# Optimization experiments

Hardware: AMD Instinct MI355X
Metric: run time of the kernel (lower is better)

Reference implementation:

```python
import jax, jax.numpy as jnp
import numpy as np

N_NODES = 100000
N_EDGES = 500000
HIDDEN = 128


def _layer_norm(h, gamma, beta, eps=1e-5):
    mu = jnp.mean(h, axis=-1, keepdims=True)
    var = jnp.var(h, axis=-1, keepdims=True)
    return (h - mu) * jax.lax.rsqrt(var + eps) * gamma + beta


def setup_inputs() -> dict:
    key = jax.random.key(0)
    ks = jax.random.split(key, 8)
    h = HIDDEN
    x = jax.random.normal(ks[0], (N_NODES, h), dtype=jnp.float32)
    edge_index = jax.random.randint(ks[1], (2, N_EDGES), 0, N_NODES, dtype=jnp.int64)
    edge = jax.random.normal(ks[2], (N_EDGES, h), dtype=jnp.float32)
    # MLP params: Linear(3h -> h), LN, SiLU, Linear(h -> h), LN, Tanh
    W1 = jax.random.normal(ks[3], (3 * h, h), dtype=jnp.float32) * (1.0 / np.sqrt(3 * h))
    b1 = jnp.zeros((h,), dtype=jnp.float32)
    g1 = jnp.ones((h,), dtype=jnp.float32)
    be1 = jnp.zeros((h,), dtype=jnp.float32)
    W2 = jax.random.normal(ks[4], (h, h), dtype=jnp.float32) * (1.0 / np.sqrt(h))
    b2 = jnp.zeros((h,), dtype=jnp.float32)
    g2 = jnp.ones((h,), dtype=jnp.float32)
    be2 = jnp.zeros((h,), dtype=jnp.float32)
    return {"x": x, "edge_index": edge_index, "edge": edge,
            "W1": W1, "b1": b1, "g1": g1, "be1": be1,
            "W2": W2, "b2": b2, "g2": g2, "be2": be2}


def reference(x, edge_index, edge, W1, b1, g1, be1, W2, b2, g2, be2):
    src = edge_index[0]
    dst = edge_index[1]
    # gather src/dst node feats, concat with edge feats -> [E, 3h]
    x_input = jnp.concatenate([x[src], x[dst], edge], axis=-1)
    h1 = jax.nn.silu(_layer_norm(x_input @ W1 + b1, g1, be1))
    h2 = jnp.tanh(_layer_norm(h1 @ W2 + b2, g2, be2))
    return edge + h2
```

## Files before the change

### kernel.cpp

```cpp
#include <hip/hip_runtime.h>

#define E_TOTAL 500000
#define NNODES  100000
#define HID     128
#define K1      384

typedef __bf16 bf16x8 __attribute__((ext_vector_type(8)));
typedef float  f32x4  __attribute__((ext_vector_type(4)));

__global__ void pack_w_kernel(const float* __restrict__ W, __bf16* __restrict__ out, int K) {
    int idx = blockIdx.x * 256 + threadIdx.x;
    if (idx >= K * 128) return;
    int k = idx >> 7, nn = idx & 127;
    int kstep = k >> 5, q = (k >> 3) & 3, j = k & 7;
    int nt = nn >> 4, n15 = nn & 15;
    int lane = q * 16 + n15;
    out[(((kstep * 8 + nt) * 64 + lane) << 3) + j] = (__bf16)W[idx];
}

__launch_bounds__(256, 2)
__global__ void edge_mlp_kernel(
    const float* __restrict__ x,
    const int*   __restrict__ eidx,
    const float* __restrict__ edge,
    const float* __restrict__ b1, const float* __restrict__ g1, const float* __restrict__ be1,
    const float* __restrict__ b2, const float* __restrict__ g2, const float* __restrict__ be2,
    const __bf16* __restrict__ w1f, const __bf16* __restrict__ w2f,
    float* __restrict__ out)
{
    __shared__ __align__(16) __bf16 h1s[4][64][128];

    const int tid  = threadIdx.x;
    const int w    = tid >> 6;
    const int l    = tid & 63;
    const int q    = l >> 4;
    const int n15  = l & 15;
    const int ebase = blockIdx.x * 256 + w * 64;

    const float* psrc[4]; const float* pdst[4]; const float* pedg[4];
    #pragma unroll
    for (int mt = 0; mt < 4; ++mt) {
        int e  = ebase + mt * 16 + n15;
        int ec = e < E_TOTAL ? e : (E_TOTAL - 1);
        int s  = eidx[ec];
        int d  = eidx[E_TOTAL + ec];
        psrc[mt] = x + (size_t)s * HID;
        pdst[mt] = x + (size_t)d * HID;
        pedg[mt] = edge + (size_t)ec * HID;
    }

    f32x4 acc[4][8];
    #pragma unroll
    for (int mt = 0; mt < 4; ++mt)
        #pragma unroll
        for (int nt = 0; nt < 8; ++nt) {
            f32x4 z = {0.f, 0.f, 0.f, 0.f};
            acc[mt][nt] = z;
        }

    #pragma unroll
    for (int ks = 0; ks < 12; ++ks) {
        bf16x8 a[4];
        #pragma unroll
        for (int mt = 0; mt < 4; ++mt) {
            const float* base =
                (ks < 4) ? (psrc[mt] + ks * 32) :
                (ks < 8) ? (pdst[mt] + (ks - 4) * 32) :
                           (pedg[mt] + (ks - 8) * 32);
            base += q * 8;
            float4 v0 = *reinterpret_cast<const float4*>(base);
            float4 v1 = *reinterpret_cast<const float4*>(base + 4);
            bf16x8 t;
            t[0]=(__bf16)v0.x; t[1]=(__bf16)v0.y; t[2]=(__bf16)v0.z; t[3]=(__bf16)v0.w;
            t[4]=(__bf16)v1.x; t[5]=(__bf16)v1.y; t[6]=(__bf16)v1.z; t[7]=(__bf16)v1.w;
            a[mt] = t;
        }
        const bf16x8* wf = reinterpret_cast<const bf16x8*>(w1f) + (size_t)(ks * 8) * 64 + l;
        #pragma unroll
        for (int nt = 0; nt < 8; ++nt) {
            bf16x8 b = wf[nt * 64];
            #pragma unroll
            for (int mt = 0; mt < 4; ++mt)
                acc[mt][nt] = __builtin_amdgcn_mfma_f32_16x16x32_bf16(a[mt], b, acc[mt][nt], 0, 0, 0);
        }
    }

    {
        float b1v[8], g1v[8], be1v[8];
        #pragma unroll
        for (int nt = 0; nt < 8; ++nt) {
            int c = nt * 16 + n15;
            b1v[nt] = b1[c]; g1v[nt] = g1[c]; be1v[nt] = be1[c];
        }
        #pragma unroll
        for (int mt = 0; mt < 4; ++mt) {
            float sm[4] = {0,0,0,0}, sq[4] = {0,0,0,0};
            #pragma unroll
            for (int nt = 0; nt < 8; ++nt)
                #pragma unroll
                for (int r = 0; r < 4; ++r) {
                    float v = acc[mt][nt][r] + b1v[nt];
                    acc[mt][nt][r] = v;
                    sm[r] += v; sq[r] += v * v;
                }
            #pragma unroll
            for (int o = 1; o < 16; o <<= 1)
                #pragma unroll
                for (int r = 0; r < 4; ++r) {
                    sm[r] += __shfl_xor(sm[r], o, 64);
                    sq[r] += __shfl_xor(sq[r], o, 64);
                }
            #pragma unroll
            for (int r = 0; r < 4; ++r) {
                float mu  = sm[r] * (1.f / 128.f);
                float var = sq[r] * (1.f / 128.f) - mu * mu;
                float rs  = rsqrtf(var + 1e-5f);
                int row = mt * 16 + q * 4 + r;
                #pragma unroll
                for (int nt = 0; nt < 8; ++nt) {
                    float v = (acc[mt][nt][r] - mu) * rs * g1v[nt] + be1v[nt];
                    float h = v * (1.f / (1.f + __expf(-v)));
                    int col = nt * 16 + n15;
                    int cb  = (col >> 3) ^ (row & 7);
                    h1s[w][row][cb * 8 + (col & 7)] = (__bf16)h;
                }
            }
        }
    }
    __syncthreads();

    #pragma unroll
    for (int mt = 0; mt < 4; ++mt)
        #pragma unroll
        for (int nt = 0; nt < 8; ++nt) {
            f32x4 z = {0.f, 0.f, 0.f, 0.f};
            acc[mt][nt] = z;
        }
    #pragma unroll
    for (int ks = 0; ks < 4; ++ks) {
        bf16x8 a[4];
        #pragma unroll
        for (int mt = 0; mt < 4; ++mt) {
            int row = mt * 16 + n15;
            int kb  = ks * 4 + q;
            int cb  = kb ^ (row & 7);
            a[mt] = *reinterpret_cast<const bf16x8*>(&h1s[w][row][cb * 8]);
        }
        const bf16x8* wf = reinterpret_cast<const bf16x8*>(w2f) + (size_t)(ks * 8) * 64 + l;
        #pragma unroll
        for (int nt = 0; nt < 8; ++nt) {
            bf16x8 b = wf[nt * 64];
            #pragma unroll
            for (int mt = 0; mt < 4; ++mt)
                acc[mt][nt] = __builtin_amdgcn_mfma_f32_16x16x32_bf16(a[mt], b, acc[mt][nt], 0, 0, 0);
        }
    }

    {
        float b2v[8], g2v[8], be2v[8];
        #pragma unroll
        for (int nt = 0; nt < 8; ++nt) {
            int c = nt * 16 + n15;
            b2v[nt] = b2[c]; g2v[nt] = g2[c]; be2v[nt] = be2[c];
        }
        #pragma unroll
        for (int mt = 0; mt < 4; ++mt) {
            float sm[4] = {0,0,0,0}, sq[4] = {0,0,0,0};
            #pragma unroll
            for (int nt = 0; nt < 8; ++nt)
                #pragma unroll
                for (int r = 0; r < 4; ++r) {
                    float v = acc[mt][nt][r] + b2v[nt];
                    acc[mt][nt][r] = v;
                    sm[r] += v; sq[r] += v * v;
                }
            #pragma unroll
            for (int o = 1; o < 16; o <<= 1)
                #pragma unroll
                for (int r = 0; r < 4; ++r) {
                    sm[r] += __shfl_xor(sm[r], o, 64);
                    sq[r] += __shfl_xor(sq[r], o, 64);
                }
            #pragma unroll
            for (int r = 0; r < 4; ++r) {
                float mu  = sm[r] * (1.f / 128.f);
                float var = sq[r] * (1.f / 128.f) - mu * mu;
                float rs  = rsqrtf(var + 1e-5f);
                int e = ebase + mt * 16 + q * 4 + r;
                if (e < E_TOTAL) {
                    #pragma unroll
                    for (int nt = 0; nt < 8; ++nt) {
                        float v = (acc[mt][nt][r] - mu) * rs * g2v[nt] + be2v[nt];
                        float tv = fminf(fmaxf(v, -15.f), 15.f);
                        float ex = __expf(2.f * tv);
                        float th = (ex - 1.f) / (ex + 1.f);
                        size_t off = (size_t)e * HID + nt * 16 + n15;
                        out[off] = edge[off] + th;
                    }
                }
            }
        }
    }
}

extern "C" void kernel_launch(void* const* d_in, const int* in_sizes, int n_in,
                              void* d_out, int out_size, void* d_ws, size_t ws_size,
                              hipStream_t stream) {
    const float* x   = (const float*)d_in[0];
    const int*   ei  = (const int*)d_in[1];
    const float* edge= (const float*)d_in[2];
    const float* W1  = (const float*)d_in[3];
    const float* b1  = (const float*)d_in[4];
    const float* g1  = (const float*)d_in[5];
    const float* be1 = (const float*)d_in[6];
    const float* W2  = (const float*)d_in[7];
    const float* b2  = (const float*)d_in[8];
    const float* g2  = (const float*)d_in[9];
    const float* be2 = (const float*)d_in[10];
    float* out = (float*)d_out;

    __bf16* w1f = (__bf16*)d_ws;
    __bf16* w2f = w1f + K1 * HID;

    pack_w_kernel<<<(K1 * HID + 255) / 256, 256, 0, stream>>>(W1, w1f, K1);
    pack_w_kernel<<<(HID * HID + 255) / 256, 256, 0, stream>>>(W2, w2f, HID);

    int nblk = (E_TOTAL + 255) / 256;
    edge_mlp_kernel<<<nblk, 256, 0, stream>>>(x, ei, edge,
                                              b1, g1, be1, b2, g2, be2,
                                              w1f, w2f, out);
}
```

Measured before the change: 657.9 us.

## Process row tiles sequentially per wave to cut registers and raise occupancy

Each wave now loops over its four 16-row tiles one at a time instead of holding all four tiles' accumulators at once. This shrinks accumulator registers and the LDS staging buffer, so launch bounds can target four blocks per CU. It also drops the block-wide barrier and writes the output with nontemporal stores. The cost is that every weight fragment is reloaded once per row tile instead of being shared across four, which roughly quadruples weight reads from cache.

```diff
diff --git a/kernel.cpp b/kernel.cpp
--- a/kernel.cpp
+++ b/kernel.cpp
@@ -18,7 +18,7 @@
     out[(((kstep * 8 + nt) * 64 + lane) << 3) + j] = (__bf16)W[idx];
 }
 
-__launch_bounds__(256, 2)
+__launch_bounds__(256, 4)
 __global__ void edge_mlp_kernel(
     const float* __restrict__ x,
     const int*   __restrict__ eidx,
@@ -28,7 +28,7 @@
     const __bf16* __restrict__ w1f, const __bf16* __restrict__ w2f,
     float* __restrict__ out)
 {
-    __shared__ __align__(16) __bf16 h1s[4][64][128];
+    __shared__ __align__(16) __bf16 h1s[4][16][128];
 
     const int tid  = threadIdx.x;
     const int w    = tid >> 6;
@@ -49,60 +49,46 @@
         pedg[mt] = edge + (size_t)ec * HID;
     }
 
-    f32x4 acc[4][8];
-    #pragma unroll
-    for (int mt = 0; mt < 4; ++mt)
+    #pragma unroll 1
+    for (int mt = 0; mt < 4; ++mt) {
+        f32x4 acc[8];
         #pragma unroll
-        for (int nt = 0; nt < 8; ++nt) {
-            f32x4 z = {0.f, 0.f, 0.f, 0.f};
-            acc[mt][nt] = z;
+        for (int nt = 0; nt < 8; ++nt) { f32x4 z = {0.f,0.f,0.f,0.f}; acc[nt] = z; }
+
+        #pragma unroll
+        for (int part = 0; part < 3; ++part) {
+            const float* base =
+                ((part == 0) ? psrc[mt] : (part == 1) ? pdst[mt] : pedg[mt]) + q * 8;
+            bf16x8 a[4];
+            #pragma unroll
+            for (int ks = 0; ks < 4; ++ks) {
+                float4 v0 = *reinterpret_cast<const float4*>(base + ks * 32);
+                float4 v1 = *reinterpret_cast<const float4*>(base + ks * 32 + 4);
+                bf16x8 t;
+                t[0]=(__bf16)v0.x; t[1]=(__bf16)v0.y; t[2]=(__bf16)v0.z; t[3]=(__bf16)v0.w;
+                t[4]=(__bf16)v1.x; t[5]=(__bf16)v1.y; t[6]=(__bf16)v1.z; t[7]=(__bf16)v1.w;
+                a[ks] = t;
+            }
+            const bf16x8* wf = reinterpret_cast<const bf16x8*>(w1f) + (size_t)(part * 32) * 64 + l;
+            #pragma unroll
+            for (int ks = 0; ks < 4; ++ks)
+                #pragma unroll
+                for (int nt = 0; nt < 8; ++nt)
+                    acc[nt] = __builtin_amdgcn_mfma_f32_16x16x32_bf16(a[ks], wf[(ks * 8 + nt) * 64], acc[nt], 0, 0, 0);
         }
 
-    #pragma unroll
-    for (int ks = 0; ks < 12; ++ks) {
-        bf16x8 a[4];
-        #pragma unroll
-        for (int mt = 0; mt < 4; ++mt) {
-            const float* base =
-                (ks < 4) ? (psrc[mt] + ks * 32) :
-                (ks < 8) ? (pdst[mt] + (ks - 4) * 32) :
-                           (pedg[mt] + (ks - 8) * 32);
-            base += q * 8;
-            float4 v0 = *reinterpret_cast<const float4*>(base);
-            float4 v1 = *reinterpret_cast<const float4*>(base + 4);
-            bf16x8 t;
-            t[0]=(__bf16)v0.x; t[1]=(__bf16)v0.y; t[2]=(__bf16)v0.z; t[3]=(__bf16)v0.w;
-            t[4]=(__bf16)v1.x; t[5]=(__bf16)v1.y; t[6]=(__bf16)v1.z; t[7]=(__bf16)v1.w;
-            a[mt] = t;
-        }
-        const bf16x8* wf = reinterpret_cast<const bf16x8*>(w1f) + (size_t)(ks * 8) * 64 + l;
-        #pragma unroll
-        for (int nt = 0; nt < 8; ++nt) {
-            bf16x8 b = wf[nt * 64];
-            #pragma unroll
-            for (int mt = 0; mt < 4; ++mt)
-                acc[mt][nt] = __builtin_amdgcn_mfma_f32_16x16x32_bf16(a[mt], b, acc[mt][nt], 0, 0, 0);
-        }
-    }
-
-    {
-        float b1v[8], g1v[8], be1v[8];
-        #pragma unroll
-        for (int nt = 0; nt < 8; ++nt) {
-            int c = nt * 16 + n15;
-            b1v[nt] = b1[c]; g1v[nt] = g1[c]; be1v[nt] = be1[c];
-        }
-        #pragma unroll
-        for (int mt = 0; mt < 4; ++mt) {
+        {
             float sm[4] = {0,0,0,0}, sq[4] = {0,0,0,0};
             #pragma unroll
-            for (int nt = 0; nt < 8; ++nt)
+            for (int nt = 0; nt < 8; ++nt) {
+                float bb = b1[nt * 16 + n15];
                 #pragma unroll
                 for (int r = 0; r < 4; ++r) {
-                    float v = acc[mt][nt][r] + b1v[nt];
-                    acc[mt][nt][r] = v;
+                    float v = acc[nt][r] + bb;
+                    acc[nt][r] = v;
                     sm[r] += v; sq[r] += v * v;
                 }
+            }
             #pragma unroll
             for (int o = 1; o < 16; o <<= 1)
                 #pragma unroll
@@ -115,65 +101,43 @@
                 float mu  = sm[r] * (1.f / 128.f);
                 float var = sq[r] * (1.f / 128.f) - mu * mu;
                 float rs  = rsqrtf(var + 1e-5f);
-                int row = mt * 16 + q * 4 + r;
+                int row = q * 4 + r;
                 #pragma unroll
                 for (int nt = 0; nt < 8; ++nt) {
-                    float v = (acc[mt][nt][r] - mu) * rs * g1v[nt] + be1v[nt];
+                    int col = nt * 16 + n15;
+                    float v = (acc[nt][r] - mu) * rs * g1[col] + be1[col];
                     float h = v * (1.f / (1.f + __expf(-v)));
-                    int col = nt * 16 + n15;
                     int cb  = (col >> 3) ^ (row & 7);
                     h1s[w][row][cb * 8 + (col & 7)] = (__bf16)h;
                 }
             }
         }
-    }
-    __syncthreads();
 
-    #pragma unroll
-    for (int mt = 0; mt < 4; ++mt)
+        f32x4 acc2[8];
         #pragma unroll
-        for (int nt = 0; nt < 8; ++nt) {
-            f32x4 z = {0.f, 0.f, 0.f, 0.f};
-            acc[mt][nt] = z;
+        for (int nt = 0; nt < 8; ++nt) { f32x4 z = {0.f,0.f,0.f,0.f}; acc2[nt] = z; }
+        #pragma unroll
+        for (int ks = 0; ks < 4; ++ks) {
+            int cb = (ks * 4 + q) ^ (n15 & 7);
+            bf16x8 a2 = *reinterpret_cast<const bf16x8*>(&h1s[w][n15][cb * 8]);
+            const bf16x8* wf = reinterpret_cast<const bf16x8*>(w2f) + (size_t)(ks * 8) * 64 + l;
+            #pragma unroll
+            for (int nt = 0; nt < 8; ++nt)
+                acc2[nt] = __builtin_amdgcn_mfma_f32_16x16x32_bf16(a2, wf[nt * 64], acc2[nt], 0, 0, 0);
         }
-    #pragma unroll
-    for (int ks = 0; ks < 4; ++ks) {
-        bf16x8 a[4];
-        #pragma unroll
-        for (int mt = 0; mt < 4; ++mt) {
-            int row = mt * 16 + n15;
-            int kb  = ks * 4 + q;
-            int cb  = kb ^ (row & 7);
-            a[mt] = *reinterpret_cast<const bf16x8*>(&h1s[w][row][cb * 8]);
-        }
-        const bf16x8* wf = reinterpret_cast<const bf16x8*>(w2f) + (size_t)(ks * 8) * 64 + l;
-        #pragma unroll
-        for (int nt = 0; nt < 8; ++nt) {
-            bf16x8 b = wf[nt * 64];
-            #pragma unroll
-            for (int mt = 0; mt < 4; ++mt)
-                acc[mt][nt] = __builtin_amdgcn_mfma_f32_16x16x32_bf16(a[mt], b, acc[mt][nt], 0, 0, 0);
-        }
-    }
 
-    {
-        float b2v[8], g2v[8], be2v[8];
-        #pragma unroll
-        for (int nt = 0; nt < 8; ++nt) {
-            int c = nt * 16 + n15;
-            b2v[nt] = b2[c]; g2v[nt] = g2[c]; be2v[nt] = be2[c];
-        }
-        #pragma unroll
-        for (int mt = 0; mt < 4; ++mt) {
+        {
             float sm[4] = {0,0,0,0}, sq[4] = {0,0,0,0};
             #pragma unroll
-            for (int nt = 0; nt < 8; ++nt)
+            for (int nt = 0; nt < 8; ++nt) {
+                float bb = b2[nt * 16 + n15];
                 #pragma unroll
                 for (int r = 0; r < 4; ++r) {
-                    float v = acc[mt][nt][r] + b2v[nt];
-                    acc[mt][nt][r] = v;
+                    float v = acc2[nt][r] + bb;
+                    acc2[nt][r] = v;
                     sm[r] += v; sq[r] += v * v;
                 }
+            }
             #pragma unroll
             for (int o = 1; o < 16; o <<= 1)
                 #pragma unroll
@@ -190,12 +154,13 @@
                 if (e < E_TOTAL) {
                     #pragma unroll
                     for (int nt = 0; nt < 8; ++nt) {
-                        float v = (acc[mt][nt][r] - mu) * rs * g2v[nt] + be2v[nt];
+                        int col = nt * 16 + n15;
+                        float v = (acc2[nt][r] - mu) * rs * g2[col] + be2[col];
                         float tv = fminf(fmaxf(v, -15.f), 15.f);
                         float ex = __expf(2.f * tv);
                         float th = (ex - 1.f) / (ex + 1.f);
-                        size_t off = (size_t)e * HID + nt * 16 + n15;
-                        out[off] = edge[off] + th;
+                        size_t off = (size_t)e * HID + col;
+                        __builtin_nontemporal_store(edge[off] + th, &out[off]);
                     }
                 }
             }
```

New measurement: 2.029 ms. 208% more time.
